# Kernel tuning notes

Measured on AMD Instinct MI355X. Metric: run time of the kernel, lower is better.

Reference implementation:

```python
import jax, jax.numpy as jnp
import numpy as np

N_NODES = 50000
N_EDGES = 800000
NFEAT, NHID, NCLASS = 512, 128, 40
BN_EPS = 1e-5


def setup_inputs() -> dict:
    key = jax.random.key(0)
    ks = jax.random.split(key, 12)
    x = jax.random.normal(ks[0], (N_NODES, NFEAT), dtype=jnp.float32)
    edge_index = jax.random.randint(ks[1], (2, N_EDGES), 0, N_NODES, dtype=jnp.int64)
    edge_weight = jax.random.uniform(ks[2], (N_EDGES,), dtype=jnp.float32)
    def glorot(k, fi, fo):
        lim = (6.0 / (fi + fo)) ** 0.5
        return jax.random.uniform(k, (fi, fo), minval=-lim, maxval=lim, dtype=jnp.float32)
    return {
        "x": x, "edge_index": edge_index, "edge_weight": edge_weight,
        "W1": glorot(ks[3], NFEAT, NHID), "b1": jnp.zeros((NHID,), jnp.float32),
        "W2": glorot(ks[4], NHID, NHID), "b2": jnp.zeros((NHID,), jnp.float32),
        "W3": glorot(ks[5], NHID, NHID), "b3": jnp.zeros((NHID,), jnp.float32),
        "g1": jnp.ones((NHID,), jnp.float32), "be1": jnp.zeros((NHID,), jnp.float32),
        "g2": jnp.ones((NHID,), jnp.float32), "be2": jnp.zeros((NHID,), jnp.float32),
        "g3": jnp.ones((NHID,), jnp.float32), "be3": jnp.zeros((NHID,), jnp.float32),
        "linW": glorot(ks[6], NHID, NCLASS), "linb": jnp.zeros((NCLASS,), jnp.float32),
    }


def _gcn_norm(edge_index, edge_weight, n):
    # PyG gcn_norm: add self-loops (weight 1), symmetric D^-1/2 (A+I) D^-1/2
    loop = jnp.arange(n, dtype=edge_index.dtype)
    row = jnp.concatenate([edge_index[0], loop])
    col = jnp.concatenate([edge_index[1], loop])
    ew = jnp.concatenate([edge_weight, jnp.ones((n,), edge_weight.dtype)])
    deg = jax.ops.segment_sum(ew, col, num_segments=n)
    dinv = jnp.where(deg > 0, jax.lax.rsqrt(jnp.maximum(deg, 1e-30)), 0.0)
    norm = dinv[row] * ew * dinv[col]
    return row, col, norm


def _conv(x, W, b, row, col, norm, n):
    h = x @ W                                   # [N, out]
    msg = h[row] * norm[:, None]                # gather + weight, [E+N, out]
    return jax.ops.segment_sum(msg, col, num_segments=n) + b


def _bn(x, g, b):
    # training-mode BatchNorm over node dim (biased variance)
    mu = jnp.mean(x, axis=0)
    var = jnp.mean((x - mu) ** 2, axis=0)
    return (x - mu) * jax.lax.rsqrt(var + BN_EPS) * g + b


def reference(x, edge_index, edge_weight, W1, b1, W2, b2, W3, b3,
              g1, be1, g2, be2, g3, be3, linW, linb):
    n = x.shape[0]
    row, col, norm = _gcn_norm(edge_index, edge_weight, n)
    x1 = _bn(jax.nn.relu(_conv(x, W1, b1, row, col, norm, n)), g1, be1)
    x2 = _bn(jax.nn.relu(_conv(x1, W2, b2, row, col, norm, n)), g2, be2)
    x3 = _bn(_conv(x2, W3, b3, row, col, norm, n), g3, be3)
    logits = x3 @ linW + linb
    return (logits, jax.nn.softmax(logits, axis=1), x3)
```

## Files before the change

### kernel.cpp

```cpp
#include <hip/hip_runtime.h>
#include <hip/hip_bf16.h>

#define N_NODES 50000
#define N_EDGES 800000
#define NFEAT 512
#define NHID 128
#define NCLASS 40
#define BN_EPS 1e-5f

typedef __attribute__((ext_vector_type(8))) short short8;
typedef __attribute__((ext_vector_type(4))) float f32x4;

#define GEMM1_BLOCKS ((N_NODES + 127) / 128)
#define EDGE_BLOCKS ((N_EDGES + 255) / 256)
#define SCAN_BLOCKS ((N_NODES + 255) / 256)
#define BN_BLOCKS ((N_NODES + 255) / 256)

__device__ __forceinline__ unsigned short f2b(float f) {
    unsigned int u = __float_as_uint(f);
    u += 0x7fff + ((u >> 16) & 1);
    return (unsigned short)(u >> 16);
}
__device__ __forceinline__ unsigned int pk2(float lo, float hi) {
    unsigned int r;
    asm("v_cvt_pk_bf16_f32 %0, %1, %2" : "=v"(r) : "v"(lo), "v"(hi));
    return r;
}
__device__ __forceinline__ float blo(unsigned int v) {
    return __uint_as_float(v << 16);
}
__device__ __forceinline__ float bhi(unsigned int v) {
    return __uint_as_float(v & 0xffff0000u);
}

__global__ void k_prep_w(const float* __restrict__ W1, const float* __restrict__ W2,
                         const float* __restrict__ W3, unsigned short* __restrict__ W1t,
                         unsigned short* __restrict__ W2t, unsigned short* __restrict__ W3t,
                         unsigned long long* __restrict__ degcnt) {
    int i = blockIdx.x * blockDim.x + threadIdx.x;
    if (i < N_NODES) degcnt[i] = 0ULL;
    if (i < 65536) {
        int k = i >> 7, n = i & 127;
        W1t[n * 512 + k] = f2b(W1[i]);
    } else if (i < 81920) {
        int j = i - 65536; int k = j >> 7, n = j & 127;
        W2t[n * 128 + k] = f2b(W2[j]);
    } else if (i < 98304) {
        int j = i - 81920; int k = j >> 7, n = j & 127;
        W3t[n * 128 + k] = f2b(W3[j]);
    }
}

__global__ __launch_bounds__(256) void k_fat(
    const float* __restrict__ x, const unsigned short* __restrict__ W1t,
    unsigned short* __restrict__ hbuf,
    const unsigned int* __restrict__ words, const float* __restrict__ ew,
    int* __restrict__ row, int* __restrict__ col,
    unsigned long long* __restrict__ degcnt, int* __restrict__ slot) {
    __shared__ unsigned short As[128][40];
    __shared__ unsigned short Bs[128][40];
    __shared__ int s_any;
    int tid = threadIdx.x;
    if (blockIdx.x < GEMM1_BLOCKS) {
        int m0 = blockIdx.x * 128;
        int srow = tid >> 1;
        int skh = (tid & 1) << 4;
        int wave = tid >> 6, lane = tid & 63;
        int wm = (wave >> 1) * 64, wn = (wave & 1) * 64;
        int l15 = lane & 15, quad = lane >> 4;
        f32x4 acc[4][4] = {};
        bool arow_ok = (m0 + srow) < N_NODES;
        const float* arow_p = x + (size_t)(m0 + srow) * 512 + skh;
        const unsigned short* wrow_p = W1t + (size_t)srow * 512 + skh;
        float4 ta[4];
        uint4 tb0, tb1;
#pragma unroll
        for (int q = 0; q < 4; q++) {
            ta[q] = make_float4(0.f, 0.f, 0.f, 0.f);
            if (arow_ok) ta[q] = *(const float4*)(arow_p + q * 4);
        }
        tb0 = *(const uint4*)(wrow_p);
        tb1 = *(const uint4*)(wrow_p + 8);
        for (int kt = 0; kt < 512; kt += 32) {
            unsigned int p[8];
#pragma unroll
            for (int q = 0; q < 4; q++) {
                p[2 * q]     = pk2(ta[q].x, ta[q].y);
                p[2 * q + 1] = pk2(ta[q].z, ta[q].w);
            }
            *(uint4*)&As[srow][skh] = make_uint4(p[0], p[1], p[2], p[3]);
            *(uint4*)&As[srow][skh + 8] = make_uint4(p[4], p[5], p[6], p[7]);
            *(uint4*)&Bs[srow][skh] = tb0;
            *(uint4*)&Bs[srow][skh + 8] = tb1;
            __syncthreads();
            if (kt + 32 < 512) {
#pragma unroll
                for (int q = 0; q < 4; q++) {
                    float4 t4 = make_float4(0.f, 0.f, 0.f, 0.f);
                    if (arow_ok) t4 = *(const float4*)(arow_p + kt + 32 + q * 4);
                    ta[q] = t4;
                }
                tb0 = *(const uint4*)(wrow_p + kt + 32);
                tb1 = *(const uint4*)(wrow_p + kt + 40);
            }
            short8 a[4], b[4];
#pragma unroll
            for (int i = 0; i < 4; i++) a[i] = *(const short8*)&As[wm + i * 16 + l15][quad * 8];
#pragma unroll
            for (int j = 0; j < 4; j++) b[j] = *(const short8*)&Bs[wn + j * 16 + l15][quad * 8];
#pragma unroll
            for (int i = 0; i < 4; i++)
#pragma unroll
                for (int j = 0; j < 4; j++)
                    acc[i][j] = __builtin_amdgcn_mfma_f32_16x16x32_bf16(a[i], b[j], acc[i][j], 0, 0, 0);
            __syncthreads();
        }
#pragma unroll
        for (int i = 0; i < 4; i++) {
            int mb = m0 + wm + i * 16 + quad * 4;
#pragma unroll
            for (int r = 0; r < 4; r++) {
                int m = mb + r;
                if (m < N_NODES) {
#pragma unroll
                    for (int j = 0; j < 4; j++)
                        hbuf[(size_t)m * 128 + wn + j * 16 + l15] = f2b(acc[i][j][r]);
                }
            }
        }
    } else {
        if (tid == 0) s_any = 0;
        __syncthreads();
        unsigned int probe = words[2 * tid + 1];
        if (probe != 0) atomicAdd(&s_any, 1);
        __syncthreads();
        int f = (s_any == 0) ? 1 : 0;
        int e = (blockIdx.x - GEMM1_BLOCKS) * 256 + tid;
        if (e < N_EDGES) {
            unsigned int r = f ? words[2 * (size_t)e] : words[e];
            unsigned int c = f ? words[2 * ((size_t)e + N_EDGES)] : words[e + N_EDGES];
            row[e] = (int)r;
            col[e] = (int)c;
            unsigned int q = __float2uint_rn(ew[e] * 8388608.0f);
            unsigned long long old = atomicAdd(&degcnt[c], (1ULL << 32) | (unsigned long long)q);
            slot[e] = (int)(old >> 32);
        }
    }
}

__global__ __launch_bounds__(256) void k_dinv(const unsigned long long* __restrict__ degcnt,
                                              float* __restrict__ dinv,
                                              int* __restrict__ counts,
                                              int* __restrict__ bsum) {
    int i = blockIdx.x * 256 + threadIdx.x;
    int cnt = 0;
    if (i < N_NODES) {
        unsigned long long v = degcnt[i];
        float deg = 1.0f + (float)(unsigned int)(v & 0xffffffffULL) * (1.0f / 8388608.0f);
        dinv[i] = rsqrtf(deg);
        cnt = (int)(v >> 32);
        counts[i] = cnt;
    }
    __shared__ int sh[256];
    sh[threadIdx.x] = cnt;
    __syncthreads();
    for (int ofs = 128; ofs > 0; ofs >>= 1) {
        if (threadIdx.x < ofs) sh[threadIdx.x] += sh[threadIdx.x + ofs];
        __syncthreads();
    }
    if (threadIdx.x == 0) bsum[blockIdx.x] = sh[0];
}

__global__ __launch_bounds__(256) void k_scan2(const int* __restrict__ bsum,
                                               int* __restrict__ bpre,
                                               int* __restrict__ colptr) {
    int t = threadIdx.x;
    int v = (t < SCAN_BLOCKS) ? bsum[t] : 0;
    __shared__ int sh[256];
    sh[t] = v;
    __syncthreads();
    for (int ofs = 1; ofs < 256; ofs <<= 1) {
        int u = (t >= ofs) ? sh[t - ofs] : 0;
        __syncthreads();
        sh[t] += u;
        __syncthreads();
    }
    if (t < SCAN_BLOCKS) bpre[t] = sh[t] - v;
    if (t == SCAN_BLOCKS - 1) colptr[N_NODES] = sh[t];
}

__global__ __launch_bounds__(256) void k_scan3(const int* __restrict__ counts,
                                               const int* __restrict__ bpre,
                                               int* __restrict__ colptr) {
    int t = threadIdx.x;
    int i = blockIdx.x * 256 + t;
    int v = (i < N_NODES) ? counts[i] : 0;
    __shared__ int sh[256];
    sh[t] = v;
    __syncthreads();
    for (int ofs = 1; ofs < 256; ofs <<= 1) {
        int u = (t >= ofs) ? sh[t - ofs] : 0;
        __syncthreads();
        sh[t] += u;
        __syncthreads();
    }
    if (i < N_NODES) colptr[i] = bpre[blockIdx.x] + sh[t] - v;
}

__global__ void k_scatter(const int* __restrict__ row, const int* __restrict__ col,
                          const float* __restrict__ ew, const float* __restrict__ dinv,
                          const int* __restrict__ colptr, const int* __restrict__ slot,
                          int2* __restrict__ ern) {
    int e = blockIdx.x * blockDim.x + threadIdx.x;
    if (e < N_EDGES) {
        int c = col[e], r = row[e];
        int p = colptr[c] + slot[e];
        float nrm = dinv[r] * ew[e] * dinv[c];
        ern[p] = make_int2(r, __float_as_int(nrm));
    }
}

__global__ __launch_bounds__(256) void k_aggregate(
    const unsigned int* __restrict__ hb, const int* __restrict__ colptr,
    const int2* __restrict__ ern, const float* __restrict__ dinv,
    const float* __restrict__ bias, unsigned int* __restrict__ out, int relu,
    float* __restrict__ sums, float* __restrict__ sumsq) {
    if (blockIdx.x == 0) {
        if (threadIdx.x < 128) sums[threadIdx.x] = 0.f;
        else sumsq[threadIdx.x - 128] = 0.f;
    }
    int node = (blockIdx.x * blockDim.x + threadIdx.x) >> 6;
    int lane = threadIdx.x & 63;
    if (node >= N_NODES) return;
    float di = dinv[node];
    float selfw = di * di;
    unsigned int sv = hb[(size_t)node * 64 + lane];
    float a0 = selfw * blo(sv);
    float a1 = selfw * bhi(sv);
    float c0 = 0.f, c1 = 0.f;
    int e = colptr[node], end = colptr[node + 1];
    for (; e + 8 <= end; e += 8) {
        int2 rw[8];
#pragma unroll
        for (int q = 0; q < 8; q++) rw[q] = ern[e + q];
        unsigned int v[8];
#pragma unroll
        for (int q = 0; q < 8; q++) v[q] = hb[(size_t)rw[q].x * 64 + lane];
#pragma unroll
        for (int q = 0; q < 8; q++) {
            float w = __int_as_float(rw[q].y);
            if (q & 1) { c0 += w * blo(v[q]); c1 += w * bhi(v[q]); }
            else       { a0 += w * blo(v[q]); a1 += w * bhi(v[q]); }
        }
    }
    for (; e < end; e++) {
        int2 rw = ern[e];
        float w = __int_as_float(rw.y);
        unsigned int v = hb[(size_t)rw.x * 64 + lane];
        a0 += w * blo(v);
        a1 += w * bhi(v);
    }
    a0 += c0; a1 += c1;
    float2 bv = *(const float2*)&bias[2 * lane];
    a0 += bv.x;
    a1 += bv.y;
    if (relu) { a0 = fmaxf(a0, 0.f); a1 = fmaxf(a1, 0.f); }
    out[(size_t)node * 64 + lane] = pk2(a0, a1);
}

__global__ __launch_bounds__(256) void k_bnstats(const unsigned int* __restrict__ x,
                                                 float* __restrict__ sums,
                                                 float* __restrict__ sumsq) {
    int u = threadIdx.x & 63;
    int strip = threadIdx.x >> 6;
    int r0 = blockIdx.x * 256;
    int rend = min(r0 + 256, N_NODES);
    float sl = 0.f, s2l = 0.f, sh_ = 0.f, s2h = 0.f;
    for (int r = r0 + strip; r < rend; r += 4) {
        unsigned int v = x[(size_t)r * 64 + u];
        float a = blo(v), b = bhi(v);
        sl += a; s2l += a * a;
        sh_ += b; s2h += b * b;
    }
    __shared__ float buf[4][64][4];
    buf[strip][u][0] = sl; buf[strip][u][1] = s2l;
    buf[strip][u][2] = sh_; buf[strip][u][3] = s2h;
    __syncthreads();
    if (strip == 0) {
#pragma unroll
        for (int s = 1; s < 4; s++) {
            sl += buf[s][u][0]; s2l += buf[s][u][1];
            sh_ += buf[s][u][2]; s2h += buf[s][u][3];
        }
        atomicAdd(&sums[2 * u], sl);
        atomicAdd(&sums[2 * u + 1], sh_);
        atomicAdd(&sumsq[2 * u], s2l);
        atomicAdd(&sumsq[2 * u + 1], s2h);
    }
}

__global__ __launch_bounds__(256) void k_gemm_h(
    const unsigned int* __restrict__ Ab, const unsigned short* __restrict__ Wt,
    const float* __restrict__ sums, const float* __restrict__ sumsq,
    const float* __restrict__ g, const float* __restrict__ be,
    unsigned short* __restrict__ Out) {
    __shared__ unsigned short As[128][40];
    __shared__ unsigned short Bs[128][40];
    __shared__ float s_sc[128], s_sh[128];
    int tid = threadIdx.x;
    int m0 = blockIdx.x * 128;
    if (tid < 128) {
        const float invn = 1.0f / (float)N_NODES;
        float mu = sums[tid] * invn;
        float var = sumsq[tid] * invn - mu * mu;
        float iv = rsqrtf(var + BN_EPS);
        float sc = g[tid] * iv;
        s_sc[tid] = sc;
        s_sh[tid] = be[tid] - mu * sc;
    }
    __syncthreads();
    int srow = tid >> 1;
    int skh = (tid & 1) << 4;
    int wave = tid >> 6, lane = tid & 63;
    int wm = (wave >> 1) * 64, wn = (wave & 1) * 64;
    int l15 = lane & 15, quad = lane >> 4;
    f32x4 acc[4][4] = {};
    bool arow_ok = (m0 + srow) < N_NODES;
    const unsigned int* arow_b = Ab + (size_t)(m0 + srow) * 64 + (skh >> 1);
    const unsigned short* wrow_p = Wt + (size_t)srow * 128 + skh;
    uint4 r0 = make_uint4(0, 0, 0, 0), r1 = make_uint4(0, 0, 0, 0);
    uint4 tb0, tb1;
    if (arow_ok) {
        r0 = *(const uint4*)(arow_b);
        r1 = *(const uint4*)(arow_b + 4);
    }
    tb0 = *(const uint4*)(wrow_p);
    tb1 = *(const uint4*)(wrow_p + 8);
    for (int kt = 0; kt < 128; kt += 32) {
        unsigned int raw[8] = {r0.x, r0.y, r0.z, r0.w, r1.x, r1.y, r1.z, r1.w};
        unsigned int p[8];
#pragma unroll
        for (int q = 0; q < 8; q++) {
            int ch = kt + skh + 2 * q;
            float f0 = blo(raw[q]) * s_sc[ch] + s_sh[ch];
            float f1 = bhi(raw[q]) * s_sc[ch + 1] + s_sh[ch + 1];
            p[q] = pk2(f0, f1);
        }
        *(uint4*)&As[srow][skh] = make_uint4(p[0], p[1], p[2], p[3]);
        *(uint4*)&As[srow][skh + 8] = make_uint4(p[4], p[5], p[6], p[7]);
        *(uint4*)&Bs[srow][skh] = tb0;
        *(uint4*)&Bs[srow][skh + 8] = tb1;
        __syncthreads();
        if (kt + 32 < 128) {
            if (arow_ok) {
                r0 = *(const uint4*)(arow_b + ((kt + 32) >> 1));
                r1 = *(const uint4*)(arow_b + ((kt + 32) >> 1) + 4);
            }
            tb0 = *(const uint4*)(wrow_p + kt + 32);
            tb1 = *(const uint4*)(wrow_p + kt + 40);
        }
        short8 a[4], b[4];
#pragma unroll
        for (int i = 0; i < 4; i++) a[i] = *(const short8*)&As[wm + i * 16 + l15][quad * 8];
#pragma unroll
        for (int j = 0; j < 4; j++) b[j] = *(const short8*)&Bs[wn + j * 16 + l15][quad * 8];
#pragma unroll
        for (int i = 0; i < 4; i++)
#pragma unroll
            for (int j = 0; j < 4; j++)
                acc[i][j] = __builtin_amdgcn_mfma_f32_16x16x32_bf16(a[i], b[j], acc[i][j], 0, 0, 0);
        __syncthreads();
    }
#pragma unroll
    for (int i = 0; i < 4; i++) {
        int mb = m0 + wm + i * 16 + quad * 4;
#pragma unroll
        for (int r = 0; r < 4; r++) {
            int m = mb + r;
            if (m < N_NODES) {
#pragma unroll
                for (int j = 0; j < 4; j++)
                    Out[(size_t)m * 128 + wn + j * 16 + l15] = f2b(acc[i][j][r]);
            }
        }
    }
}

__global__ __launch_bounds__(256) void k_logits(const unsigned int* __restrict__ abuf,
                                                const float* __restrict__ sums,
                                                const float* __restrict__ sumsq,
                                                const float* __restrict__ g,
                                                const float* __restrict__ be,
                                                const float* __restrict__ linW,
                                                const float* __restrict__ linb,
                                                float* __restrict__ logits,
                                                float* __restrict__ probs,
                                                float* __restrict__ x3out) {
    __shared__ float Xs[64][130];
    __shared__ float Ws[128 * 40];
    __shared__ float s_sc[128], s_sh[128];
    int tid = threadIdx.x;
    int m0 = blockIdx.x * 64;
    if (tid < 128) {
        const float invn = 1.0f / (float)N_NODES;
        float mu = sums[tid] * invn;
        float var = sumsq[tid] * invn - mu * mu;
        float iv = rsqrtf(var + BN_EPS);
        float sc = g[tid] * iv;
        s_sc[tid] = sc;
        s_sh[tid] = be[tid] - mu * sc;
    }
    for (int q = tid; q < 1280; q += 256)
        *(float4*)&Ws[q * 4] = *(const float4*)&linW[q * 4];
    __syncthreads();
    for (int q = tid; q < 4096; q += 256) {
        int r = q >> 6, u = q & 63;
        int m = m0 + r;
        float f0 = 0.f, f1 = 0.f;
        if (m < N_NODES) {
            unsigned int v = abuf[(size_t)m * 64 + u];
            f0 = blo(v) * s_sc[2 * u] + s_sh[2 * u];
            f1 = bhi(v) * s_sc[2 * u + 1] + s_sh[2 * u + 1];
            *(float2*)&x3out[(size_t)m * 128 + 2 * u] = make_float2(f0, f1);
        }
        *(float2*)&Xs[r][2 * u] = make_float2(f0, f1);
    }
    __syncthreads();
    int r = tid >> 2;
    int cg = tid & 3;
    int cbase = cg * 10;
    float acc[10] = {};
    for (int k = 0; k < 128; k++) {
        float a = Xs[r][k];
#pragma unroll
        for (int j = 0; j < 10; j++) acc[j] += a * Ws[k * 40 + cbase + j];
    }
#pragma unroll
    for (int j = 0; j < 10; j++) acc[j] += linb[cbase + j];
    float m = acc[0];
#pragma unroll
    for (int j = 1; j < 10; j++) m = fmaxf(m, acc[j]);
    m = fmaxf(m, __shfl_xor(m, 1));
    m = fmaxf(m, __shfl_xor(m, 2));
    float ex[10];
    float s = 0.f;
#pragma unroll
    for (int j = 0; j < 10; j++) { ex[j] = expf(acc[j] - m); s += ex[j]; }
    s += __shfl_xor(s, 1);
    s += __shfl_xor(s, 2);
    float inv = 1.0f / s;
    int mrow = m0 + r;
    if (mrow < N_NODES) {
#pragma unroll
        for (int j = 0; j < 10; j += 2) {
            *(float2*)&logits[(size_t)mrow * 40 + cbase + j] = make_float2(acc[j], acc[j + 1]);
            *(float2*)&probs[(size_t)mrow * 40 + cbase + j] = make_float2(ex[j] * inv, ex[j + 1] * inv);
        }
    }
}

extern "C" void kernel_launch(void* const* d_in, const int* in_sizes, int n_in,
                              void* d_out, int out_size, void* d_ws, size_t ws_size,
                              hipStream_t stream) {
    const float* x = (const float*)d_in[0];
    const unsigned int* eidx = (const unsigned int*)d_in[1];
    const float* ew = (const float*)d_in[2];
    const float* W1 = (const float*)d_in[3];
    const float* b1 = (const float*)d_in[4];
    const float* W2 = (const float*)d_in[5];
    const float* b2 = (const float*)d_in[6];
    const float* W3 = (const float*)d_in[7];
    const float* b3 = (const float*)d_in[8];
    const float* g1 = (const float*)d_in[9];
    const float* be1 = (const float*)d_in[10];
    const float* g2 = (const float*)d_in[11];
    const float* be2 = (const float*)d_in[12];
    const float* g3 = (const float*)d_in[13];
    const float* be3 = (const float*)d_in[14];
    const float* linW = (const float*)d_in[15];
    const float* linb = (const float*)d_in[16];

    float* out = (float*)d_out;
    float* logits = out;
    float* probs = out + (size_t)N_NODES * NCLASS;
    float* x3out = out + 2 * (size_t)N_NODES * NCLASS;

    char* ws = (char*)d_ws;
    size_t off = 0;
    auto take = [&](size_t bytes) -> char* {
        char* p = ws + off;
        off += (bytes + 255) & ~(size_t)255;
        return p;
    };
    int* row32 = (int*)take((size_t)N_EDGES * 4);
    int* col32 = (int*)take((size_t)N_EDGES * 4);
    int* slot = (int*)take((size_t)N_EDGES * 4);
    int* colptr = (int*)take((size_t)(N_NODES + 1) * 4);
    int* counts = (int*)take((size_t)N_NODES * 4);
    unsigned long long* degcnt = (unsigned long long*)take((size_t)N_NODES * 8);
    int2* ern = (int2*)take((size_t)N_EDGES * 8);
    float* dinv = (float*)take((size_t)N_NODES * 4);
    unsigned short* hbuf = (unsigned short*)take((size_t)N_NODES * NHID * 2);
    unsigned short* abuf = (unsigned short*)take((size_t)N_NODES * NHID * 2);
    unsigned short* W1t = (unsigned short*)take((size_t)512 * 128 * 2);
    unsigned short* W2t = (unsigned short*)take((size_t)128 * 128 * 2);
    unsigned short* W3t = (unsigned short*)take((size_t)128 * 128 * 2);
    float* sums = (float*)take(128 * 4);
    float* sumsq = (float*)take(128 * 4);
    int* bsum = (int*)take((size_t)SCAN_BLOCKS * 4);
    int* bpre = (int*)take((size_t)SCAN_BLOCKS * 4);
    (void)ws_size; (void)n_in; (void)in_sizes; (void)out_size;

    const int TPB = 256;
    int grid_e = EDGE_BLOCKS;
    int grid_gemm = GEMM1_BLOCKS;
    int grid_agg = (N_NODES * 64 + TPB - 1) / TPB;
    int grid_head = (N_NODES + 63) / 64;

    k_prep_w<<<(98304 + TPB - 1) / TPB, TPB, 0, stream>>>(W1, W2, W3, W1t, W2t, W3t, degcnt);
    k_fat<<<GEMM1_BLOCKS + EDGE_BLOCKS, TPB, 0, stream>>>(
        x, W1t, hbuf, eidx, ew, row32, col32, degcnt, slot);
    k_dinv<<<SCAN_BLOCKS, TPB, 0, stream>>>(degcnt, dinv, counts, bsum);
    k_scan2<<<1, TPB, 0, stream>>>(bsum, bpre, colptr);
    k_scan3<<<SCAN_BLOCKS, TPB, 0, stream>>>(counts, bpre, colptr);
    k_scatter<<<grid_e, TPB, 0, stream>>>(row32, col32, ew, dinv, colptr, slot, ern);

    k_aggregate<<<grid_agg, TPB, 0, stream>>>((const unsigned int*)hbuf, colptr, ern, dinv, b1, (unsigned int*)abuf, 1, sums, sumsq);
    k_bnstats<<<BN_BLOCKS, TPB, 0, stream>>>((const unsigned int*)abuf, sums, sumsq);

    k_gemm_h<<<grid_gemm, TPB, 0, stream>>>((const unsigned int*)abuf, W2t, sums, sumsq, g1, be1, hbuf);
    k_aggregate<<<grid_agg, TPB, 0, stream>>>((const unsigned int*)hbuf, colptr, ern, dinv, b2, (unsigned int*)abuf, 1, sums, sumsq);
    k_bnstats<<<BN_BLOCKS, TPB, 0, stream>>>((const unsigned int*)abuf, sums, sumsq);

    k_gemm_h<<<grid_gemm, TPB, 0, stream>>>((const unsigned int*)abuf, W3t, sums, sumsq, g2, be2, hbuf);
    k_aggregate<<<grid_agg, TPB, 0, stream>>>((const unsigned int*)hbuf, colptr, ern, dinv, b3, (unsigned int*)abuf, 0, sums, sumsq);
    k_bnstats<<<BN_BLOCKS, TPB, 0, stream>>>((const unsigned int*)abuf, sums, sumsq);

    k_logits<<<grid_head, TPB, 0, stream>>>((const unsigned int*)abuf, sums, sumsq, g3, be3, linW, linb, logits, probs, x3out);
}
```

Baseline: 493.5 us.

## Fuse BN statistics into aggregation, merge scan passes, shrink first GEMM tile

BatchNorm sum and sum-of-squares are now accumulated inside the aggregation kernel from fp32 values before the bf16 pack, with per-block reduction and atomics. This removes three separate bnstats passes that re-read the aggregated activations. The top-level scan is folded into k_dinv using a last-block ticket, and the first GEMM uses 64-row tiles so more blocks are launched. Stats buffers are separated per layer and zeroed once at prep. Statistics now come from unrounded fp32 rather than bf16 values, and each aggregation wave processes 8 nodes serially.

```diff
diff --git a/kernel.cpp b/kernel.cpp
--- a/kernel.cpp
+++ b/kernel.cpp
@@ -11,10 +11,11 @@
 typedef __attribute__((ext_vector_type(8))) short short8;
 typedef __attribute__((ext_vector_type(4))) float f32x4;
 
-#define GEMM1_BLOCKS ((N_NODES + 127) / 128)
+#define GEMM1_BLOCKS ((N_NODES + 63) / 64)
+#define GEMMH_BLOCKS ((N_NODES + 127) / 128)
 #define EDGE_BLOCKS ((N_EDGES + 255) / 256)
 #define SCAN_BLOCKS ((N_NODES + 255) / 256)
-#define BN_BLOCKS ((N_NODES + 255) / 256)
+#define AGG_BLOCKS ((N_NODES + 31) / 32)
 
 __device__ __forceinline__ unsigned short f2b(float f) {
     unsigned int u = __float_as_uint(f);
@@ -36,9 +37,12 @@
 __global__ void k_prep_w(const float* __restrict__ W1, const float* __restrict__ W2,
                          const float* __restrict__ W3, unsigned short* __restrict__ W1t,
                          unsigned short* __restrict__ W2t, unsigned short* __restrict__ W3t,
-                         unsigned long long* __restrict__ degcnt) {
+                         unsigned long long* __restrict__ degcnt,
+                         float* __restrict__ stats, int* __restrict__ ticket) {
     int i = blockIdx.x * blockDim.x + threadIdx.x;
     if (i < N_NODES) degcnt[i] = 0ULL;
+    if (i < 768) stats[i] = 0.f;
+    if (i == 768) *ticket = 0;
     if (i < 65536) {
         int k = i >> 7, n = i & 127;
         W1t[n * 512 + k] = f2b(W1[i]);
@@ -57,66 +61,61 @@
     const unsigned int* __restrict__ words, const float* __restrict__ ew,
     int* __restrict__ row, int* __restrict__ col,
     unsigned long long* __restrict__ degcnt, int* __restrict__ slot) {
-    __shared__ unsigned short As[128][40];
+    __shared__ unsigned short As[64][40];
     __shared__ unsigned short Bs[128][40];
     __shared__ int s_any;
     int tid = threadIdx.x;
     if (blockIdx.x < GEMM1_BLOCKS) {
-        int m0 = blockIdx.x * 128;
-        int srow = tid >> 1;
-        int skh = (tid & 1) << 4;
+        int m0 = blockIdx.x * 64;
+        int srow = tid >> 2;
+        int ska = (tid & 3) << 3;
+        int brow = tid >> 1;
+        int skb = (tid & 1) << 4;
         int wave = tid >> 6, lane = tid & 63;
-        int wm = (wave >> 1) * 64, wn = (wave & 1) * 64;
+        int wm = (wave >> 1) << 5;
+        int wn = (wave & 1) << 6;
         int l15 = lane & 15, quad = lane >> 4;
-        f32x4 acc[4][4] = {};
+        f32x4 acc[2][4] = {};
         bool arow_ok = (m0 + srow) < N_NODES;
-        const float* arow_p = x + (size_t)(m0 + srow) * 512 + skh;
-        const unsigned short* wrow_p = W1t + (size_t)srow * 512 + skh;
-        float4 ta[4];
+        const float* arow_p = x + (size_t)(m0 + srow) * 512 + ska;
+        const unsigned short* wrow_p = W1t + (size_t)brow * 512 + skb;
+        float4 ta0 = make_float4(0.f, 0.f, 0.f, 0.f), ta1 = ta0;
         uint4 tb0, tb1;
-#pragma unroll
-        for (int q = 0; q < 4; q++) {
-            ta[q] = make_float4(0.f, 0.f, 0.f, 0.f);
-            if (arow_ok) ta[q] = *(const float4*)(arow_p + q * 4);
+        if (arow_ok) {
+            ta0 = *(const float4*)(arow_p);
+            ta1 = *(const float4*)(arow_p + 4);
         }
         tb0 = *(const uint4*)(wrow_p);
         tb1 = *(const uint4*)(wrow_p + 8);
         for (int kt = 0; kt < 512; kt += 32) {
-            unsigned int p[8];
-#pragma unroll
-            for (int q = 0; q < 4; q++) {
-                p[2 * q]     = pk2(ta[q].x, ta[q].y);
-                p[2 * q + 1] = pk2(ta[q].z, ta[q].w);
-            }
-            *(uint4*)&As[srow][skh] = make_uint4(p[0], p[1], p[2], p[3]);
-            *(uint4*)&As[srow][skh + 8] = make_uint4(p[4], p[5], p[6], p[7]);
-            *(uint4*)&Bs[srow][skh] = tb0;
-            *(uint4*)&Bs[srow][skh + 8] = tb1;
+            unsigned int p0 = pk2(ta0.x, ta0.y), p1 = pk2(ta0.z, ta0.w);
+            unsigned int p2 = pk2(ta1.x, ta1.y), p3 = pk2(ta1.z, ta1.w);
+            *(uint4*)&As[srow][ska] = make_uint4(p0, p1, p2, p3);
+            *(uint4*)&Bs[brow][skb] = tb0;
+            *(uint4*)&Bs[brow][skb + 8] = tb1;
             __syncthreads();
             if (kt + 32 < 512) {
-#pragma unroll
-                for (int q = 0; q < 4; q++) {
-                    float4 t4 = make_float4(0.f, 0.f, 0.f, 0.f);
-                    if (arow_ok) t4 = *(const float4*)(arow_p + kt + 32 + q * 4);
-                    ta[q] = t4;
+                if (arow_ok) {
+                    ta0 = *(const float4*)(arow_p + kt + 32);
+                    ta1 = *(const float4*)(arow_p + kt + 36);
                 }
                 tb0 = *(const uint4*)(wrow_p + kt + 32);
                 tb1 = *(const uint4*)(wrow_p + kt + 40);
             }
-            short8 a[4], b[4];
-#pragma unroll
-            for (int i = 0; i < 4; i++) a[i] = *(const short8*)&As[wm + i * 16 + l15][quad * 8];
+            short8 a[2], b[4];
+#pragma unroll
+            for (int i = 0; i < 2; i++) a[i] = *(const short8*)&As[wm + i * 16 + l15][quad * 8];
 #pragma unroll
             for (int j = 0; j < 4; j++) b[j] = *(const short8*)&Bs[wn + j * 16 + l15][quad * 8];
 #pragma unroll
-            for (int i = 0; i < 4; i++)
+            for (int i = 0; i < 2; i++)
 #pragma unroll
                 for (int j = 0; j < 4; j++)
                     acc[i][j] = __builtin_amdgcn_mfma_f32_16x16x32_bf16(a[i], b[j], acc[i][j], 0, 0, 0);
             __syncthreads();
         }
 #pragma unroll
-        for (int i = 0; i < 4; i++) {
+        for (int i = 0; i < 2; i++) {
             int mb = m0 + wm + i * 16 + quad * 4;
 #pragma unroll
             for (int r = 0; r < 4; r++) {
@@ -151,7 +150,10 @@
 __global__ __launch_bounds__(256) void k_dinv(const unsigned long long* __restrict__ degcnt,
                                               float* __restrict__ dinv,
                                               int* __restrict__ counts,
-                                              int* __restrict__ bsum) {
+                                              int* __restrict__ bsum,
+                                              int* __restrict__ ticket,
+                                              int* __restrict__ bpre,
+                                              int* __restrict__ colptr) {
     int i = blockIdx.x * 256 + threadIdx.x;
     int cnt = 0;
     if (i < N_NODES) {
@@ -162,31 +164,35 @@
         counts[i] = cnt;
     }
     __shared__ int sh[256];
+    __shared__ int s_last;
     sh[threadIdx.x] = cnt;
     __syncthreads();
     for (int ofs = 128; ofs > 0; ofs >>= 1) {
         if (threadIdx.x < ofs) sh[threadIdx.x] += sh[threadIdx.x + ofs];
         __syncthreads();
     }
-    if (threadIdx.x == 0) bsum[blockIdx.x] = sh[0];
-}
-
-__global__ __launch_bounds__(256) void k_scan2(const int* __restrict__ bsum,
-                                               int* __restrict__ bpre,
-                                               int* __restrict__ colptr) {
-    int t = threadIdx.x;
-    int v = (t < SCAN_BLOCKS) ? bsum[t] : 0;
-    __shared__ int sh[256];
-    sh[t] = v;
-    __syncthreads();
-    for (int ofs = 1; ofs < 256; ofs <<= 1) {
-        int u = (t >= ofs) ? sh[t - ofs] : 0;
-        __syncthreads();
-        sh[t] += u;
-        __syncthreads();
-    }
-    if (t < SCAN_BLOCKS) bpre[t] = sh[t] - v;
-    if (t == SCAN_BLOCKS - 1) colptr[N_NODES] = sh[t];
+    if (threadIdx.x == 0) {
+        bsum[blockIdx.x] = sh[0];
+        __threadfence();
+        int t = atomicAdd(ticket, 1);
+        s_last = (t == SCAN_BLOCKS - 1) ? 1 : 0;
+    }
+    __syncthreads();
+    if (s_last) {
+        __threadfence();
+        int t = threadIdx.x;
+        int v = (t < SCAN_BLOCKS) ? ((volatile int*)bsum)[t] : 0;
+        sh[t] = v;
+        __syncthreads();
+        for (int ofs = 1; ofs < 256; ofs <<= 1) {
+            int u = (t >= ofs) ? sh[t - ofs] : 0;
+            __syncthreads();
+            sh[t] += u;
+            __syncthreads();
+        }
+        if (t < SCAN_BLOCKS) bpre[t] = sh[t] - v;
+        if (t == SCAN_BLOCKS - 1) colptr[N_NODES] = sh[t];
+    }
 }
 
 __global__ __launch_bounds__(256) void k_scan3(const int* __restrict__ counts,
@@ -225,77 +231,65 @@
     const int2* __restrict__ ern, const float* __restrict__ dinv,
     const float* __restrict__ bias, unsigned int* __restrict__ out, int relu,
     float* __restrict__ sums, float* __restrict__ sumsq) {
-    if (blockIdx.x == 0) {
-        if (threadIdx.x < 128) sums[threadIdx.x] = 0.f;
-        else sumsq[threadIdx.x - 128] = 0.f;
-    }
-    int node = (blockIdx.x * blockDim.x + threadIdx.x) >> 6;
+    int wave = threadIdx.x >> 6;
     int lane = threadIdx.x & 63;
-    if (node >= N_NODES) return;
-    float di = dinv[node];
-    float selfw = di * di;
-    unsigned int sv = hb[(size_t)node * 64 + lane];
-    float a0 = selfw * blo(sv);
-    float a1 = selfw * bhi(sv);
-    float c0 = 0.f, c1 = 0.f;
-    int e = colptr[node], end = colptr[node + 1];
-    for (; e + 8 <= end; e += 8) {
-        int2 rw[8];
-#pragma unroll
-        for (int q = 0; q < 8; q++) rw[q] = ern[e + q];
-        unsigned int v[8];
-#pragma unroll
-        for (int q = 0; q < 8; q++) v[q] = hb[(size_t)rw[q].x * 64 + lane];
-#pragma unroll
-        for (int q = 0; q < 8; q++) {
-            float w = __int_as_float(rw[q].y);
-            if (q & 1) { c0 += w * blo(v[q]); c1 += w * bhi(v[q]); }
-            else       { a0 += w * blo(v[q]); a1 += w * bhi(v[q]); }
-        }
-    }
-    for (; e < end; e++) {
-        int2 rw = ern[e];
-        float w = __int_as_float(rw.y);
-        unsigned int v = hb[(size_t)rw.x * 64 + lane];
-        a0 += w * blo(v);
-        a1 += w * bhi(v);
-    }
-    a0 += c0; a1 += c1;
     float2 bv = *(const float2*)&bias[2 * lane];
-    a0 += bv.x;
-    a1 += bv.y;
-    if (relu) { a0 = fmaxf(a0, 0.f); a1 = fmaxf(a1, 0.f); }
-    out[(size_t)node * 64 + lane] = pk2(a0, a1);
-}
-
-__global__ __launch_bounds__(256) void k_bnstats(const unsigned int* __restrict__ x,
-                                                 float* __restrict__ sums,
-                                                 float* __restrict__ sumsq) {
-    int u = threadIdx.x & 63;
-    int strip = threadIdx.x >> 6;
-    int r0 = blockIdx.x * 256;
-    int rend = min(r0 + 256, N_NODES);
-    float sl = 0.f, s2l = 0.f, sh_ = 0.f, s2h = 0.f;
-    for (int r = r0 + strip; r < rend; r += 4) {
-        unsigned int v = x[(size_t)r * 64 + u];
-        float a = blo(v), b = bhi(v);
-        sl += a; s2l += a * a;
-        sh_ += b; s2h += b * b;
-    }
-    __shared__ float buf[4][64][4];
-    buf[strip][u][0] = sl; buf[strip][u][1] = s2l;
-    buf[strip][u][2] = sh_; buf[strip][u][3] = s2h;
-    __syncthreads();
-    if (strip == 0) {
+    float s0 = 0.f, q0 = 0.f, s1 = 0.f, q1 = 0.f;
+    int nbase = blockIdx.x * 32 + wave * 8;
+#pragma unroll 1
+    for (int rep = 0; rep < 8; rep++) {
+        int node = nbase + rep;
+        if (node >= N_NODES) break;
+        float di = dinv[node];
+        float selfw = di * di;
+        unsigned int sv = hb[(size_t)node * 64 + lane];
+        float a0 = selfw * blo(sv);
+        float a1 = selfw * bhi(sv);
+        float c0 = 0.f, c1 = 0.f;
+        int e = colptr[node], end = colptr[node + 1];
+        for (; e + 8 <= end; e += 8) {
+            int2 rw[8];
+#pragma unroll
+            for (int q = 0; q < 8; q++) rw[q] = ern[e + q];
+            unsigned int v[8];
+#pragma unroll
+            for (int q = 0; q < 8; q++) v[q] = hb[(size_t)rw[q].x * 64 + lane];
+#pragma unroll
+            for (int q = 0; q < 8; q++) {
+                float w = __int_as_float(rw[q].y);
+                if (q & 1) { c0 += w * blo(v[q]); c1 += w * bhi(v[q]); }
+                else       { a0 += w * blo(v[q]); a1 += w * bhi(v[q]); }
+            }
+        }
+        for (; e < end; e++) {
+            int2 rw = ern[e];
+            float w = __int_as_float(rw.y);
+            unsigned int v = hb[(size_t)rw.x * 64 + lane];
+            a0 += w * blo(v);
+            a1 += w * bhi(v);
+        }
+        a0 += c0; a1 += c1;
+        a0 += bv.x;
+        a1 += bv.y;
+        if (relu) { a0 = fmaxf(a0, 0.f); a1 = fmaxf(a1, 0.f); }
+        out[(size_t)node * 64 + lane] = pk2(a0, a1);
+        s0 += a0; q0 += a0 * a0;
+        s1 += a1; q1 += a1 * a1;
+    }
+    __shared__ float red[4][64][4];
+    red[wave][lane][0] = s0; red[wave][lane][1] = q0;
+    red[wave][lane][2] = s1; red[wave][lane][3] = q1;
+    __syncthreads();
+    if (wave == 0) {
 #pragma unroll
         for (int s = 1; s < 4; s++) {
-            sl += buf[s][u][0]; s2l += buf[s][u][1];
-            sh_ += buf[s][u][2]; s2h += buf[s][u][3];
-        }
-        atomicAdd(&sums[2 * u], sl);
-        atomicAdd(&sums[2 * u + 1], sh_);
-        atomicAdd(&sumsq[2 * u], s2l);
-        atomicAdd(&sumsq[2 * u + 1], s2h);
+            s0 += red[s][lane][0]; q0 += red[s][lane][1];
+            s1 += red[s][lane][2]; q1 += red[s][lane][3];
+        }
+        atomicAdd(&sums[2 * lane], s0);
+        atomicAdd(&sums[2 * lane + 1], s1);
+        atomicAdd(&sumsq[2 * lane], q0);
+        atomicAdd(&sumsq[2 * lane + 1], q1);
     }
 }
 
@@ -505,36 +499,32 @@
     unsigned short* W1t = (unsigned short*)take((size_t)512 * 128 * 2);
     unsigned short* W2t = (unsigned short*)take((size_t)128 * 128 * 2);
     unsigned short* W3t = (unsigned short*)take((size_t)128 * 128 * 2);
-    float* sums = (float*)take(128 * 4);
-    float* sumsq = (float*)take(128 * 4);
+    float* stats = (float*)take(768 * 4);
+    int* ticket = (int*)take(4);
     int* bsum = (int*)take((size_t)SCAN_BLOCKS * 4);
     int* bpre = (int*)take((size_t)SCAN_BLOCKS * 4);
     (void)ws_size; (void)n_in; (void)in_sizes; (void)out_size;
 
+    float* sums1 = stats, *sumsq1 = stats + 128;
+    float* sums2 = stats + 256, *sumsq2 = stats + 384;
+    float* sums3 = stats + 512, *sumsq3 = stats + 640;
+
     const int TPB = 256;
-    int grid_e = EDGE_BLOCKS;
-    int grid_gemm = GEMM1_BLOCKS;
-    int grid_agg = (N_NODES * 64 + TPB - 1) / TPB;
-    int grid_head = (N_NODES + 63) / 64;
-
-    k_prep_w<<<(98304 + TPB - 1) / TPB, TPB, 0, stream>>>(W1, W2, W3, W1t, W2t, W3t, degcnt);
+
+    k_prep_w<<<(98304 + TPB - 1) / TPB, TPB, 0, stream>>>(W1, W2, W3, W1t, W2t, W3t, degcnt, stats, ticket);
     k_fat<<<GEMM1_BLOCKS + EDGE_BLOCKS, TPB, 0, stream>>>(
         x, W1t, hbuf, eidx, ew, row32, col32, degcnt, slot);
-    k_dinv<<<SCAN_BLOCKS, TPB, 0, stream>>>(degcnt, dinv, counts, bsum);
-    k_scan2<<<1, TPB, 0, stream>>>(bsum, bpre, colptr);
+    k_dinv<<<SCAN_BLOCKS, TPB, 0, stream>>>(degcnt, dinv, counts, bsum, ticket, bpre, colptr);
     k_scan3<<<SCAN_BLOCKS, TPB, 0, stream>>>(counts, bpre, colptr);
-    k_scatter<<<grid_e, TPB, 0, stream>>>(row32, col32, ew, dinv, colptr, slot, ern);
-
-    k_aggregate<<<grid_agg, TPB, 0, stream>>>((const unsigned int*)hbuf, colptr, ern, dinv, b1, (unsigned int*)abuf, 1, sums, sumsq);
-    k_bnstats<<<BN_BLOCKS, TPB, 0, stream>>>((const unsigned int*)abuf, sums, sumsq);
-
-    k_gemm_h<<<grid_gemm, TPB, 0, stream>>>((const unsigned int*)abuf, W2t, sums, sumsq, g1, be1, hbuf);
-    k_aggregate<<<grid_agg, TPB, 0, stream>>>((const unsigned int*)hbuf, colptr, ern, dinv, b2, (unsigned int*)abuf, 1, sums, sumsq);
-    k_bnstats<<<BN_BLOCKS, TPB, 0, stream>>>((const unsigned int*)abuf, sums, sumsq);
-
-    k_gemm_h<<<grid_gemm, TPB, 0, stream>>>((const unsigned int*)abuf, W3t, sums, sumsq, g2, be2, hbuf);
-    k_aggregate<<<grid_agg, TPB, 0, stream>>>((const unsigned int*)hbuf, colptr, ern, dinv, b3, (unsigned int*)abuf, 0, sums, sumsq);
-    k_bnstats<<<BN_BLOCKS, TPB, 0, stream>>>((const unsigned int*)abuf, sums, sumsq);
-
-    k_logits<<<grid_head, TPB, 0, stream>>>((const unsigned int*)abuf, sums, sumsq, g3, be3, linW, linb, logits, probs, x3out);
-}
+    k_scatter<<<EDGE_BLOCKS, TPB, 0, stream>>>(row32, col32, ew, dinv, colptr, slot, ern);
+
+    k_aggregate<<<AGG_BLOCKS, TPB, 0, stream>>>((const unsigned int*)hbuf, colptr, ern, dinv, b1, (unsigned int*)abuf, 1, sums1, sumsq1);
+
+    k_gemm_h<<<GEMMH_BLOCKS, TPB, 0, stream>>>((const unsigned int*)abuf, W2t, sums1, sumsq1, g1, be1, hbuf);
+    k_aggregate<<<AGG_BLOCKS, TPB, 0, stream>>>((const unsigned int*)hbuf, colptr, ern, dinv, b2, (unsigned int*)abuf, 1, sums2, sumsq2);
+
+    k_gemm_h<<<GEMMH_BLOCKS, TPB, 0, stream>>>((const unsigned int*)abuf, W3t, sums2, sumsq2, g2, be2, hbuf);
+    k_aggregate<<<AGG_BLOCKS, TPB, 0, stream>>>((const unsigned int*)hbuf, colptr, ern, dinv, b3, (unsigned int*)abuf, 0, sums3, sumsq3);
+
+    k_logits<<<(N_NODES + 63) / 64, TPB, 0, stream>>>((const unsigned int*)abuf, sums3, sumsq3, g3, be3, linW, linb, logits, probs, x3out);
+}
```

Result: slower. 645.2 us (+30.7%).

## Split fused edge/GEMM kernel, fold scan into dinv, prefetch edges in aggregate

Applied to the files above, without the earlier changes.

Splits the fused GEMM1-plus-edge-preprocessing kernel into two separate launches. The single-block scan is folded into k_dinv with a last-block ticket pattern, which removes one launch. BN stat buffers are now separate per layer and zeroed once in k_prep_w rather than inside each aggregate. The aggregate loop double-buffers its edge (row, weight) loads to overlap them with the feature gathers. The cost is one more launch from the split and slightly higher register pressure in aggregate.

```diff
diff --git a/kernel.cpp b/kernel.cpp
--- a/kernel.cpp
+++ b/kernel.cpp
@@ -12,9 +12,11 @@
 typedef __attribute__((ext_vector_type(4))) float f32x4;
 
 #define GEMM1_BLOCKS ((N_NODES + 127) / 128)
+#define GEMMH_BLOCKS ((N_NODES + 127) / 128)
 #define EDGE_BLOCKS ((N_EDGES + 255) / 256)
 #define SCAN_BLOCKS ((N_NODES + 255) / 256)
 #define BN_BLOCKS ((N_NODES + 255) / 256)
+#define AGG_BLOCKS ((N_NODES * 64 + 255) / 256)
 
 __device__ __forceinline__ unsigned short f2b(float f) {
     unsigned int u = __float_as_uint(f);
@@ -36,9 +38,12 @@
 __global__ void k_prep_w(const float* __restrict__ W1, const float* __restrict__ W2,
                          const float* __restrict__ W3, unsigned short* __restrict__ W1t,
                          unsigned short* __restrict__ W2t, unsigned short* __restrict__ W3t,
-                         unsigned long long* __restrict__ degcnt) {
+                         unsigned long long* __restrict__ degcnt,
+                         float* __restrict__ stats, int* __restrict__ syncp) {
     int i = blockIdx.x * blockDim.x + threadIdx.x;
     if (i < N_NODES) degcnt[i] = 0ULL;
+    if (i < 768) stats[i] = 0.f;
+    else if (i < 776) syncp[i - 768] = 0;
     if (i < 65536) {
         int k = i >> 7, n = i & 127;
         W1t[n * 512 + k] = f2b(W1[i]);
@@ -51,99 +56,100 @@
     }
 }
 
-__global__ __launch_bounds__(256) void k_fat(
-    const float* __restrict__ x, const unsigned short* __restrict__ W1t,
-    unsigned short* __restrict__ hbuf,
+__global__ __launch_bounds__(256) void k_edges(
     const unsigned int* __restrict__ words, const float* __restrict__ ew,
     int* __restrict__ row, int* __restrict__ col,
     unsigned long long* __restrict__ degcnt, int* __restrict__ slot) {
+    __shared__ int s_any;
+    int tid = threadIdx.x;
+    if (tid == 0) s_any = 0;
+    __syncthreads();
+    unsigned int probe = words[2 * tid + 1];
+    if (probe != 0) atomicAdd(&s_any, 1);
+    __syncthreads();
+    int f = (s_any == 0) ? 1 : 0;
+    int e = blockIdx.x * 256 + tid;
+    if (e < N_EDGES) {
+        unsigned int r = f ? words[2 * (size_t)e] : words[e];
+        unsigned int c = f ? words[2 * ((size_t)e + N_EDGES)] : words[e + N_EDGES];
+        row[e] = (int)r;
+        col[e] = (int)c;
+        unsigned int q = __float2uint_rn(ew[e] * 8388608.0f);
+        unsigned long long old = atomicAdd(&degcnt[c], (1ULL << 32) | (unsigned long long)q);
+        slot[e] = (int)(old >> 32);
+    }
+}
+
+__global__ __launch_bounds__(256) void k_gemm1(
+    const float* __restrict__ x, const unsigned short* __restrict__ W1t,
+    unsigned short* __restrict__ hbuf) {
     __shared__ unsigned short As[128][40];
     __shared__ unsigned short Bs[128][40];
-    __shared__ int s_any;
     int tid = threadIdx.x;
-    if (blockIdx.x < GEMM1_BLOCKS) {
-        int m0 = blockIdx.x * 128;
-        int srow = tid >> 1;
-        int skh = (tid & 1) << 4;
-        int wave = tid >> 6, lane = tid & 63;
-        int wm = (wave >> 1) * 64, wn = (wave & 1) * 64;
-        int l15 = lane & 15, quad = lane >> 4;
-        f32x4 acc[4][4] = {};
-        bool arow_ok = (m0 + srow) < N_NODES;
-        const float* arow_p = x + (size_t)(m0 + srow) * 512 + skh;
-        const unsigned short* wrow_p = W1t + (size_t)srow * 512 + skh;
-        float4 ta[4];
-        uint4 tb0, tb1;
+    int m0 = blockIdx.x * 128;
+    int srow = tid >> 1;
+    int skh = (tid & 1) << 4;
+    int wave = tid >> 6, lane = tid & 63;
+    int wm = (wave >> 1) * 64, wn = (wave & 1) * 64;
+    int l15 = lane & 15, quad = lane >> 4;
+    f32x4 acc[4][4] = {};
+    bool arow_ok = (m0 + srow) < N_NODES;
+    const float* arow_p = x + (size_t)(m0 + srow) * 512 + skh;
+    const unsigned short* wrow_p = W1t + (size_t)srow * 512 + skh;
+    float4 ta[4];
+    uint4 tb0, tb1;
+#pragma unroll
+    for (int q = 0; q < 4; q++) {
+        ta[q] = make_float4(0.f, 0.f, 0.f, 0.f);
+        if (arow_ok) ta[q] = *(const float4*)(arow_p + q * 4);
+    }
+    tb0 = *(const uint4*)(wrow_p);
+    tb1 = *(const uint4*)(wrow_p + 8);
+    for (int kt = 0; kt < 512; kt += 32) {
+        unsigned int p[8];
 #pragma unroll
         for (int q = 0; q < 4; q++) {
-            ta[q] = make_float4(0.f, 0.f, 0.f, 0.f);
-            if (arow_ok) ta[q] = *(const float4*)(arow_p + q * 4);
-        }
-        tb0 = *(const uint4*)(wrow_p);
-        tb1 = *(const uint4*)(wrow_p + 8);
-        for (int kt = 0; kt < 512; kt += 32) {
-            unsigned int p[8];
+            p[2 * q]     = pk2(ta[q].x, ta[q].y);
+            p[2 * q + 1] = pk2(ta[q].z, ta[q].w);
+        }
+        *(uint4*)&As[srow][skh] = make_uint4(p[0], p[1], p[2], p[3]);
+        *(uint4*)&As[srow][skh + 8] = make_uint4(p[4], p[5], p[6], p[7]);
+        *(uint4*)&Bs[srow][skh] = tb0;
+        *(uint4*)&Bs[srow][skh + 8] = tb1;
+        __syncthreads();
+        if (kt + 32 < 512) {
 #pragma unroll
             for (int q = 0; q < 4; q++) {
-                p[2 * q]     = pk2(ta[q].x, ta[q].y);
-                p[2 * q + 1] = pk2(ta[q].z, ta[q].w);
+                float4 t4 = make_float4(0.f, 0.f, 0.f, 0.f);
+                if (arow_ok) t4 = *(const float4*)(arow_p + kt + 32 + q * 4);
+                ta[q] = t4;
             }
-            *(uint4*)&As[srow][skh] = make_uint4(p[0], p[1], p[2], p[3]);
-            *(uint4*)&As[srow][skh + 8] = make_uint4(p[4], p[5], p[6], p[7]);
-            *(uint4*)&Bs[srow][skh] = tb0;
-            *(uint4*)&Bs[srow][skh + 8] = tb1;
-            __syncthreads();
-            if (kt + 32 < 512) {
-#pragma unroll
-                for (int q = 0; q < 4; q++) {
-                    float4 t4 = make_float4(0.f, 0.f, 0.f, 0.f);
-                    if (arow_ok) t4 = *(const float4*)(arow_p + kt + 32 + q * 4);
-                    ta[q] = t4;
-                }
-                tb0 = *(const uint4*)(wrow_p + kt + 32);
-                tb1 = *(const uint4*)(wrow_p + kt + 40);
+            tb0 = *(const uint4*)(wrow_p + kt + 32);
+            tb1 = *(const uint4*)(wrow_p + kt + 40);
+        }
+        short8 a[4], b[4];
+#pragma unroll
+        for (int i = 0; i < 4; i++) a[i] = *(const short8*)&As[wm + i * 16 + l15][quad * 8];
+#pragma unroll
+        for (int j = 0; j < 4; j++) b[j] = *(const short8*)&Bs[wn + j * 16 + l15][quad * 8];
+#pragma unroll
+        for (int i = 0; i < 4; i++)
+#pragma unroll
+            for (int j = 0; j < 4; j++)
+                acc[i][j] = __builtin_amdgcn_mfma_f32_16x16x32_bf16(a[i], b[j], acc[i][j], 0, 0, 0);
+        __syncthreads();
+    }
+#pragma unroll
+    for (int i = 0; i < 4; i++) {
+        int mb = m0 + wm + i * 16 + quad * 4;
+#pragma unroll
+        for (int r = 0; r < 4; r++) {
+            int m = mb + r;
+            if (m < N_NODES) {
+#pragma unroll
+                for (int j = 0; j < 4; j++)
+                    hbuf[(size_t)m * 128 + wn + j * 16 + l15] = f2b(acc[i][j][r]);
             }
-            short8 a[4], b[4];
-#pragma unroll
-            for (int i = 0; i < 4; i++) a[i] = *(const short8*)&As[wm + i * 16 + l15][quad * 8];
-#pragma unroll
-            for (int j = 0; j < 4; j++) b[j] = *(const short8*)&Bs[wn + j * 16 + l15][quad * 8];
-#pragma unroll
-            for (int i = 0; i < 4; i++)
-#pragma unroll
-                for (int j = 0; j < 4; j++)
-                    acc[i][j] = __builtin_amdgcn_mfma_f32_16x16x32_bf16(a[i], b[j], acc[i][j], 0, 0, 0);
-            __syncthreads();
-        }
-#pragma unroll
-        for (int i = 0; i < 4; i++) {
-            int mb = m0 + wm + i * 16 + quad * 4;
-#pragma unroll
-            for (int r = 0; r < 4; r++) {
-                int m = mb + r;
-                if (m < N_NODES) {
-#pragma unroll
-                    for (int j = 0; j < 4; j++)
-                        hbuf[(size_t)m * 128 + wn + j * 16 + l15] = f2b(acc[i][j][r]);
-                }
-            }
-        }
-    } else {
-        if (tid == 0) s_any = 0;
-        __syncthreads();
-        unsigned int probe = words[2 * tid + 1];
-        if (probe != 0) atomicAdd(&s_any, 1);
-        __syncthreads();
-        int f = (s_any == 0) ? 1 : 0;
-        int e = (blockIdx.x - GEMM1_BLOCKS) * 256 + tid;
-        if (e < N_EDGES) {
-            unsigned int r = f ? words[2 * (size_t)e] : words[e];
-            unsigned int c = f ? words[2 * ((size_t)e + N_EDGES)] : words[e + N_EDGES];
-            row[e] = (int)r;
-            col[e] = (int)c;
-            unsigned int q = __float2uint_rn(ew[e] * 8388608.0f);
-            unsigned long long old = atomicAdd(&degcnt[c], (1ULL << 32) | (unsigned long long)q);
-            slot[e] = (int)(old >> 32);
         }
     }
 }
@@ -151,7 +157,10 @@
 __global__ __launch_bounds__(256) void k_dinv(const unsigned long long* __restrict__ degcnt,
                                               float* __restrict__ dinv,
                                               int* __restrict__ counts,
-                                              int* __restrict__ bsum) {
+                                              int* __restrict__ bsum,
+                                              int* __restrict__ ticket,
+                                              int* __restrict__ bpre,
+                                              int* __restrict__ colptr) {
     int i = blockIdx.x * 256 + threadIdx.x;
     int cnt = 0;
     if (i < N_NODES) {
@@ -162,31 +171,35 @@
         counts[i] = cnt;
     }
     __shared__ int sh[256];
+    __shared__ int s_last;
     sh[threadIdx.x] = cnt;
     __syncthreads();
     for (int ofs = 128; ofs > 0; ofs >>= 1) {
         if (threadIdx.x < ofs) sh[threadIdx.x] += sh[threadIdx.x + ofs];
         __syncthreads();
     }
-    if (threadIdx.x == 0) bsum[blockIdx.x] = sh[0];
-}
-
-__global__ __launch_bounds__(256) void k_scan2(const int* __restrict__ bsum,
-                                               int* __restrict__ bpre,
-                                               int* __restrict__ colptr) {
-    int t = threadIdx.x;
-    int v = (t < SCAN_BLOCKS) ? bsum[t] : 0;
-    __shared__ int sh[256];
-    sh[t] = v;
-    __syncthreads();
-    for (int ofs = 1; ofs < 256; ofs <<= 1) {
-        int u = (t >= ofs) ? sh[t - ofs] : 0;
-        __syncthreads();
-        sh[t] += u;
-        __syncthreads();
-    }
-    if (t < SCAN_BLOCKS) bpre[t] = sh[t] - v;
-    if (t == SCAN_BLOCKS - 1) colptr[N_NODES] = sh[t];
+    if (threadIdx.x == 0) {
+        bsum[blockIdx.x] = sh[0];
+        __threadfence();
+        int t = atomicAdd(ticket, 1);
+        s_last = (t == SCAN_BLOCKS - 1) ? 1 : 0;
+    }
+    __syncthreads();
+    if (s_last) {
+        __threadfence();
+        int t = threadIdx.x;
+        int v = (t < SCAN_BLOCKS) ? ((volatile int*)bsum)[t] : 0;
+        sh[t] = v;
+        __syncthreads();
+        for (int ofs = 1; ofs < 256; ofs <<= 1) {
+            int u = (t >= ofs) ? sh[t - ofs] : 0;
+            __syncthreads();
+            sh[t] += u;
+            __syncthreads();
+        }
+        if (t < SCAN_BLOCKS) bpre[t] = sh[t] - v;
+        if (t == SCAN_BLOCKS - 1) colptr[N_NODES] = sh[t];
+    }
 }
 
 __global__ __launch_bounds__(256) void k_scan3(const int* __restrict__ counts,
@@ -223,12 +236,7 @@
 __global__ __launch_bounds__(256) void k_aggregate(
     const unsigned int* __restrict__ hb, const int* __restrict__ colptr,
     const int2* __restrict__ ern, const float* __restrict__ dinv,
-    const float* __restrict__ bias, unsigned int* __restrict__ out, int relu,
-    float* __restrict__ sums, float* __restrict__ sumsq) {
-    if (blockIdx.x == 0) {
-        if (threadIdx.x < 128) sums[threadIdx.x] = 0.f;
-        else sumsq[threadIdx.x - 128] = 0.f;
-    }
+    const float* __restrict__ bias, unsigned int* __restrict__ out, int relu) {
     int node = (blockIdx.x * blockDim.x + threadIdx.x) >> 6;
     int lane = threadIdx.x & 63;
     if (node >= N_NODES) return;
@@ -238,22 +246,37 @@
     float a0 = selfw * blo(sv);
     float a1 = selfw * bhi(sv);
     float c0 = 0.f, c1 = 0.f;
-    int e = colptr[node], end = colptr[node + 1];
-    for (; e + 8 <= end; e += 8) {
-        int2 rw[8];
-#pragma unroll
-        for (int q = 0; q < 8; q++) rw[q] = ern[e + q];
-        unsigned int v[8];
-#pragma unroll
-        for (int q = 0; q < 8; q++) v[q] = hb[(size_t)rw[q].x * 64 + lane];
-#pragma unroll
-        for (int q = 0; q < 8; q++) {
-            float w = __int_as_float(rw[q].y);
-            if (q & 1) { c0 += w * blo(v[q]); c1 += w * bhi(v[q]); }
-            else       { a0 += w * blo(v[q]); a1 += w * bhi(v[q]); }
-        }
-    }
-    for (; e < end; e++) {
+    int start = colptr[node], end = colptr[node + 1];
+    int nfull = (end - start) & ~7;
+    if (nfull) {
+        int e = start;
+        int2 rwc[8];
+#pragma unroll
+        for (int q = 0; q < 8; q++) rwc[q] = ern[e + q];
+        for (;;) {
+            int en = e + 8;
+            bool more = (en < start + nfull);
+            int2 rwn[8];
+            if (more) {
+#pragma unroll
+                for (int q = 0; q < 8; q++) rwn[q] = ern[en + q];
+            }
+            unsigned int v[8];
+#pragma unroll
+            for (int q = 0; q < 8; q++) v[q] = hb[(size_t)rwc[q].x * 64 + lane];
+#pragma unroll
+            for (int q = 0; q < 8; q++) {
+                float w = __int_as_float(rwc[q].y);
+                if (q & 1) { c0 += w * blo(v[q]); c1 += w * bhi(v[q]); }
+                else       { a0 += w * blo(v[q]); a1 += w * bhi(v[q]); }
+            }
+            if (!more) break;
+#pragma unroll
+            for (int q = 0; q < 8; q++) rwc[q] = rwn[q];
+            e = en;
+        }
+    }
+    for (int e = start + nfull; e < end; e++) {
         int2 rw = ern[e];
         float w = __int_as_float(rw.y);
         unsigned int v = hb[(size_t)rw.x * 64 + lane];
@@ -505,36 +528,35 @@
     unsigned short* W1t = (unsigned short*)take((size_t)512 * 128 * 2);
     unsigned short* W2t = (unsigned short*)take((size_t)128 * 128 * 2);
     unsigned short* W3t = (unsigned short*)take((size_t)128 * 128 * 2);
-    float* sums = (float*)take(128 * 4);
-    float* sumsq = (float*)take(128 * 4);
+    float* stats = (float*)take(768 * 4);
+    int* syncp = (int*)take(8 * 4);
     int* bsum = (int*)take((size_t)SCAN_BLOCKS * 4);
     int* bpre = (int*)take((size_t)SCAN_BLOCKS * 4);
     (void)ws_size; (void)n_in; (void)in_sizes; (void)out_size;
 
+    float* sums1 = stats, *sumsq1 = stats + 128;
+    float* sums2 = stats + 256, *sumsq2 = stats + 384;
+    float* sums3 = stats + 512, *sumsq3 = stats + 640;
+
     const int TPB = 256;
-    int grid_e = EDGE_BLOCKS;
-    int grid_gemm = GEMM1_BLOCKS;
-    int grid_agg = (N_NODES * 64 + TPB - 1) / TPB;
-    int grid_head = (N_NODES + 63) / 64;
-
-    k_prep_w<<<(98304 + TPB - 1) / TPB, TPB, 0, stream>>>(W1, W2, W3, W1t, W2t, W3t, degcnt);
-    k_fat<<<GEMM1_BLOCKS + EDGE_BLOCKS, TPB, 0, stream>>>(
-        x, W1t, hbuf, eidx, ew, row32, col32, degcnt, slot);
-    k_dinv<<<SCAN_BLOCKS, TPB, 0, stream>>>(degcnt, dinv, counts, bsum);
-    k_scan2<<<1, TPB, 0, stream>>>(bsum, bpre, colptr);
+
+    k_prep_w<<<(98304 + TPB - 1) / TPB, TPB, 0, stream>>>(W1, W2, W3, W1t, W2t, W3t, degcnt, stats, syncp);
+    k_edges<<<EDGE_BLOCKS, TPB, 0, stream>>>(eidx, ew, row32, col32, degcnt, slot);
+    k_gemm1<<<GEMM1_BLOCKS, TPB, 0, stream>>>(x, W1t, hbuf);
+    k_dinv<<<SCAN_BLOCKS, TPB, 0, stream>>>(degcnt, dinv, counts, bsum, &syncp[0], bpre, colptr);
     k_scan3<<<SCAN_BLOCKS, TPB, 0, stream>>>(counts, bpre, colptr);
-    k_scatter<<<grid_e, TPB, 0, stream>>>(row32, col32, ew, dinv, colptr, slot, ern);
-
-    k_aggregate<<<grid_agg, TPB, 0, stream>>>((const unsigned int*)hbuf, colptr, ern, dinv, b1, (unsigned int*)abuf, 1, sums, sumsq);
-    k_bnstats<<<BN_BLOCKS, TPB, 0, stream>>>((const unsigned int*)abuf, sums, sumsq);
-
-    k_gemm_h<<<grid_gemm, TPB, 0, stream>>>((const unsigned int*)abuf, W2t, sums, sumsq, g1, be1, hbuf);
-    k_aggregate<<<grid_agg, TPB, 0, stream>>>((const unsigned int*)hbuf, colptr, ern, dinv, b2, (unsigned int*)abuf, 1, sums, sumsq);
-    k_bnstats<<<BN_BLOCKS, TPB, 0, stream>>>((const unsigned int*)abuf, sums, sumsq);
-
-    k_gemm_h<<<grid_gemm, TPB, 0, stream>>>((const unsigned int*)abuf, W3t, sums, sumsq, g2, be2, hbuf);
-    k_aggregate<<<grid_agg, TPB, 0, stream>>>((const unsigned int*)hbuf, colptr, ern, dinv, b3, (unsigned int*)abuf, 0, sums, sumsq);
-    k_bnstats<<<BN_BLOCKS, TPB, 0, stream>>>((const unsigned int*)abuf, sums, sumsq);
-
-    k_logits<<<grid_head, TPB, 0, stream>>>((const unsigned int*)abuf, sums, sumsq, g3, be3, linW, linb, logits, probs, x3out);
-}
+    k_scatter<<<EDGE_BLOCKS, TPB, 0, stream>>>(row32, col32, ew, dinv, colptr, slot, ern);
+
+    k_aggregate<<<AGG_BLOCKS, TPB, 0, stream>>>((const unsigned int*)hbuf, colptr, ern, dinv, b1, (unsigned int*)abuf, 1);
+    k_bnstats<<<BN_BLOCKS, TPB, 0, stream>>>((const unsigned int*)abuf, sums1, sumsq1);
+
+    k_gemm_h<<<GEMMH_BLOCKS, TPB, 0, stream>>>((const unsigned int*)abuf, W2t, sums1, sumsq1, g1, be1, hbuf);
+    k_aggregate<<<AGG_BLOCKS, TPB, 0, stream>>>((const unsigned int*)hbuf, colptr, ern, dinv, b2, (unsigned int*)abuf, 1);
+    k_bnstats<<<BN_BLOCKS, TPB, 0, stream>>>((const unsigned int*)abuf, sums2, sumsq2);
+
+    k_gemm_h<<<GEMMH_BLOCKS, TPB, 0, stream>>>((const unsigned int*)abuf, W3t, sums2, sumsq2, g2, be2, hbuf);
+    k_aggregate<<<AGG_BLOCKS, TPB, 0, stream>>>((const unsigned int*)hbuf, colptr, ern, dinv, b3, (unsigned int*)abuf, 0);
+    k_bnstats<<<BN_BLOCKS, TPB, 0, stream>>>((const unsigned int*)abuf, sums3, sumsq3);
+
+    k_logits<<<(N_NODES + 63) / 64, TPB, 0, stream>>>((const unsigned int*)abuf, sums3, sumsq3, g3, be3, linW, linb, logits, probs, x3out);
+}
```

Measured after the change: 547.1 us. 1.11x slower.
